# Kernel tuning notes

Hardware: AMD Instinct MI355X
Metric: run time of the kernel (lower is better)

The kernel has to match this reference:

```python
import jax, jax.numpy as jnp
import numpy as np

BN_EPS = 1e-5


def setup_inputs() -> dict:
    key = jax.random.key(0)
    ks = jax.random.split(key, 6)
    b, c_out, c_high = 8, 256, 512
    h1 = w1 = 64
    h2 = w2 = 32
    return {
        "fms_low": jax.random.normal(ks[0], (b, c_out, h1, w1), jnp.float32),
        "fms_high": jax.random.normal(ks[1], (b, c_high, h2, w2), jnp.float32),
        "w_conv": jax.random.normal(ks[2], (c_out, c_high), jnp.float32) * (1.0 / np.sqrt(c_high)),
        "bn_gamma": jnp.ones((c_out,), jnp.float32),
        "bn_beta": jnp.zeros((c_out,), jnp.float32),
        "bn_mean": jnp.zeros((c_out,), jnp.float32),
        "bn_var": jnp.ones((c_out,), jnp.float32),
        "fc1_w": jax.random.normal(ks[3], (c_out // 4, c_out), jnp.float32) * (1.0 / np.sqrt(c_out)),
        "fc1_b": jnp.zeros((c_out // 4,), jnp.float32),
        "fc2_w": jax.random.normal(ks[4], (c_out // 4, c_out), jnp.float32) * (1.0 / np.sqrt(c_out)),
        "fc2_b": jnp.zeros((c_out // 4,), jnp.float32),
        "scale": jax.random.normal(ks[5], (1,), jnp.float32),
    }


def reference(fms_low, fms_high, w_conv, bn_gamma, bn_beta, bn_mean, bn_var,
              fc1_w, fc1_b, fc2_w, fc2_b, scale):
    b, c, h1, w1 = fms_low.shape
    # conv_high: 1x1 conv (no bias) + BN (inference) + ReLU
    x = jnp.einsum('bchw,oc->bohw', fms_high, w_conv)  # [b, 256, h2, w2]
    inv = bn_gamma / jnp.sqrt(bn_var + BN_EPS)
    x = x * inv[None, :, None, None] + (bn_beta - bn_mean * inv)[None, :, None, None]
    x = jax.nn.relu(x)
    # raw row-major reshapes, matching torch .view(b, -1, C)
    feat_low = fms_low.reshape(b, -1, c)    # [b, N_low, 256]
    feat_high = x.reshape(b, -1, c)         # [b, N_high, 256]
    mid_low = feat_low @ fc1_w.T + fc1_b    # [b, N_low, 64]
    mid_high = feat_high @ fc2_w.T + fc2_b  # [b, N_high, 64]
    energy = jnp.einsum('bnd,bmd->bnm', mid_low, mid_high)  # [b, N_low, N_high]
    attn = jax.nn.softmax(energy, axis=-1)
    # bmm(feat_high^T, attn^T) -> [b, 256, N_low]
    mid = jnp.einsum('bmc,bnm->bcn', feat_high, attn).reshape(b, c, h1, w1)
    return scale[0] * mid
```

## Files before the change

kernel.cpp:

```cpp
#include <hip/hip_runtime.h>
#include <hip/hip_bf16.h>

typedef __bf16 v8bf __attribute__((ext_vector_type(8)));
typedef float  v4f  __attribute__((ext_vector_type(4)));

typedef __attribute__((address_space(3))) void       lds_vd;
typedef __attribute__((address_space(1))) const void gbl_vd;

#define MFMA16(a, b, c) __builtin_amdgcn_mfma_f32_16x16x32_bf16(a, b, c, 0, 0, 0)

__device__ __forceinline__ void split_hl(float v, __bf16* h, __bf16* l) {
    __bf16 hh = (__bf16)v;
    *h = hh;
    *l = (__bf16)(v - (float)hh);
}

__device__ __forceinline__ int swz_idx(int row, int col) {
    return row * 64 + ((((col >> 3) ^ (row & 7))) << 3) + (col & 7);
}
__device__ __forceinline__ const __bf16* frag_ptr(const __bf16* base, int row, int g) {
    return base + row * 64 + ((g ^ (row & 7)) << 3);
}


__global__ __launch_bounds__(256) void k_conv(
    const float* __restrict__ FH, const float* __restrict__ W,
    const float* __restrict__ gamma, const float* __restrict__ beta,
    const float* __restrict__ mean, const float* __restrict__ var,
    __bf16* __restrict__ Xhi, __bf16* __restrict__ Xlo, __bf16* __restrict__ VT)
{
    __shared__ __align__(16) __bf16 Ah[64 * 64];
    __shared__ __align__(16) __bf16 Al[64 * 64];
    __shared__ __align__(16) __bf16 Bh[64 * 64];
    __shared__ __align__(16) __bf16 Bl[64 * 64];
    __shared__ float invl[64], shl[64];

    const int tid = threadIdx.x, lane = tid & 63, w = tid >> 6;
    const int l15 = lane & 15, quad = lane >> 4;
    const int u0 = blockIdx.x * 16, o0 = blockIdx.y * 64, b = blockIdx.z;
    const float* FHb = FH + (size_t)b * 524288;

    if (tid < 64) {
        const int o = o0 + tid;
        const float iv = gamma[o] * rsqrtf(var[o] + 1e-5f);
        invl[tid] = iv;
        shl[tid] = beta[o] - mean[o] * iv;
    }

    const int ao = tid >> 2, aseg = tid & 3;
    float wreg[16], freg[16];
    {
        const float* wp = W + (size_t)(o0 + ao) * 512 + aseg * 16;
        #pragma unroll
        for (int q = 0; q < 4; ++q) {
            float4 f = ((const float4*)wp)[q];
            wreg[4*q] = f.x; wreg[4*q+1] = f.y; wreg[4*q+2] = f.z; wreg[4*q+3] = f.w;
        }
        const float* fp = FHb + (size_t)lane * 1024 + w * 256 + u0;
        #pragma unroll
        for (int q = 0; q < 4; ++q) {
            float4 f = ((const float4*)fp)[q];
            freg[4*q] = f.x; freg[4*q+1] = f.y; freg[4*q+2] = f.z; freg[4*q+3] = f.w;
        }
    }

    v4f acc[2][2];
    #pragma unroll
    for (int i = 0; i < 2; ++i)
        #pragma unroll
        for (int j = 0; j < 2; ++j) { v4f z = {0.f,0.f,0.f,0.f}; acc[i][j] = z; }
    const int oh = w >> 1, nh = w & 1;

    for (int ch = 0; ch < 8; ++ch) {
        if (ch) __syncthreads();
        #pragma unroll
        for (int z = 0; z < 2; ++z) {
            v8bf hv, lv;
            #pragma unroll
            for (int e = 0; e < 8; ++e) {
                __bf16 h, l; split_hl(wreg[8*z + e], &h, &l);
                hv[e] = h; lv[e] = l;
            }
            const int gi = (2*aseg + z) ^ (ao & 7);
            *(v8bf*)(Ah + ao*64 + (gi << 3)) = hv;
            *(v8bf*)(Al + ao*64 + (gi << 3)) = lv;
        }
        #pragma unroll
        for (int ul = 0; ul < 16; ++ul) {
            __bf16 h, l; split_hl(freg[ul], &h, &l);
            const int idx = (w*16 + ul)*64 + (((lane >> 3) ^ (ul & 7)) << 3) + (lane & 7);
            Bh[idx] = h; Bl[idx] = l;
        }
        __syncthreads();
        if (ch < 7) {
            const int c1 = (ch + 1) * 64;
            const float* wp = W + (size_t)(o0 + ao) * 512 + c1 + aseg * 16;
            #pragma unroll
            for (int q = 0; q < 4; ++q) {
                float4 f = ((const float4*)wp)[q];
                wreg[4*q] = f.x; wreg[4*q+1] = f.y; wreg[4*q+2] = f.z; wreg[4*q+3] = f.w;
            }
            const float* fp = FHb + (size_t)(c1 + lane) * 1024 + w * 256 + u0;
            #pragma unroll
            for (int q = 0; q < 4; ++q) {
                float4 f = ((const float4*)fp)[q];
                freg[4*q] = f.x; freg[4*q+1] = f.y; freg[4*q+2] = f.z; freg[4*q+3] = f.w;
            }
        }
        #pragma unroll
        for (int ks = 0; ks < 2; ++ks) {
            const int g = 4*ks + quad;
            v8bf a_h[2], a_l[2], b_h[2], b_l[2];
            #pragma unroll
            for (int i = 0; i < 2; ++i) {
                const int row = oh*32 + i*16 + l15;
                a_h[i] = *(const v8bf*)frag_ptr(Ah, row, g);
                a_l[i] = *(const v8bf*)frag_ptr(Al, row, g);
            }
            #pragma unroll
            for (int j = 0; j < 2; ++j) {
                const int row = nh*32 + j*16 + l15;
                b_h[j] = *(const v8bf*)frag_ptr(Bh, row, g);
                b_l[j] = *(const v8bf*)frag_ptr(Bl, row, g);
            }
            #pragma unroll
            for (int i = 0; i < 2; ++i)
                #pragma unroll
                for (int j = 0; j < 2; ++j) {
                    acc[i][j] = MFMA16(a_h[i], b_h[j], acc[i][j]);
                    acc[i][j] = MFMA16(a_h[i], b_l[j], acc[i][j]);
                    acc[i][j] = MFMA16(a_l[i], b_h[j], acc[i][j]);
                }
        }
    }
    __syncthreads();

    #pragma unroll
    for (int i = 0; i < 2; ++i)
        #pragma unroll
        for (int j = 0; j < 2; ++j)
            #pragma unroll
            for (int r = 0; r < 4; ++r) {
                const int row = oh*32 + i*16 + quad*4 + r;
                const int col = nh*32 + j*16 + l15;
                float v = acc[i][j][r] * invl[row] + shl[row];
                v = fmaxf(v, 0.f);
                __bf16 h, l; split_hl(v, &h, &l);
                const int idx = swz_idx(row, col);
                Ah[idx] = h; Al[idx] = l;
            }
    __syncthreads();
    {
        const int o = tid >> 2, pv = tid & 3;
        const size_t gbase = ((size_t)b*256 + o0 + o) * 1024 + pv*256 + u0;
        #pragma unroll
        for (int z = 0; z < 2; ++z) {
            const int gi = (2*pv + z) ^ (o & 7);
            v8bf h = *(v8bf*)(Ah + o*64 + (gi << 3));
            v8bf l = *(v8bf*)(Al + o*64 + (gi << 3));
            *(v8bf*)(Xhi + gbase + z*8) = h;
            *(v8bf*)(Xlo + gbase + z*8) = l;
        }
    }
    {
        const int ul = tid >> 4, s = tid & 15;
        __bf16 tmp[16];
        #pragma unroll
        for (int k = 0; k < 16; ++k) {
            const int m = s*16 + k;
            const int row = m >> 2;
            const int col = (m & 3)*16 + ul;
            tmp[k] = Ah[swz_idx(row, col)];
        }
        __bf16* vp = VT + ((size_t)b*256 + u0 + ul) * 1024 + 4*o0 + s*16;
        *(v8bf*)(vp)     = *(v8bf*)(tmp);
        *(v8bf*)(vp + 8) = *(v8bf*)(tmp + 8);
    }
}

__global__ __launch_bounds__(256) void k_proj32(
    const float* __restrict__ Feat, const float* __restrict__ Wfc,
    const float* __restrict__ bfc,
    __bf16* __restrict__ Ohi, __bf16* __restrict__ Olo)
{
    __shared__ __align__(16) __bf16 Ah[128 * 64], Al[128 * 64];
    __shared__ __align__(16) __bf16 Bh[64 * 64],  Bl[64 * 64];
    const int tid = threadIdx.x, lane = tid & 63, w = tid >> 6;
    const int l15 = lane & 15, quad = lane >> 4;
    const int r0 = blockIdx.x * 128;
    const int arow = tid >> 1, ahalf = tid & 1;
    const int brow = tid >> 2, bseg = tid & 3;

    float areg[32], breg[16];
    {
        const float* ap = Feat + (size_t)(r0 + arow) * 256 + ahalf * 32;
        #pragma unroll
        for (int q = 0; q < 8; ++q) {
            float4 f = ((const float4*)ap)[q];
            areg[4*q] = f.x; areg[4*q+1] = f.y; areg[4*q+2] = f.z; areg[4*q+3] = f.w;
        }
        const float* bp = Wfc + (size_t)brow * 256 + bseg * 16;
        #pragma unroll
        for (int q = 0; q < 4; ++q) {
            float4 f = ((const float4*)bp)[q];
            breg[4*q] = f.x; breg[4*q+1] = f.y; breg[4*q+2] = f.z; breg[4*q+3] = f.w;
        }
    }
    v4f acc[2][4];
    #pragma unroll
    for (int i = 0; i < 2; ++i)
        #pragma unroll
        for (int j = 0; j < 4; ++j) { v4f z = {0.f,0.f,0.f,0.f}; acc[i][j] = z; }

    for (int ch = 0; ch < 4; ++ch) {
        if (ch) __syncthreads();
        #pragma unroll
        for (int z = 0; z < 4; ++z) {
            v8bf hv, lv;
            #pragma unroll
            for (int e = 0; e < 8; ++e) {
                __bf16 h, l; split_hl(areg[8*z + e], &h, &l);
                hv[e] = h; lv[e] = l;
            }
            const int gi = (4*ahalf + z) ^ (arow & 7);
            *(v8bf*)(Ah + arow*64 + (gi << 3)) = hv;
            *(v8bf*)(Al + arow*64 + (gi << 3)) = lv;
        }
        #pragma unroll
        for (int z = 0; z < 2; ++z) {
            v8bf hv, lv;
            #pragma unroll
            for (int e = 0; e < 8; ++e) {
                __bf16 h, l; split_hl(breg[8*z + e], &h, &l);
                hv[e] = h; lv[e] = l;
            }
            const int gi = (2*bseg + z) ^ (brow & 7);
            *(v8bf*)(Bh + brow*64 + (gi << 3)) = hv;
            *(v8bf*)(Bl + brow*64 + (gi << 3)) = lv;
        }
        __syncthreads();
        if (ch < 3) {
            const int c1 = (ch + 1) * 64;
            const float* ap = Feat + (size_t)(r0 + arow) * 256 + c1 + ahalf * 32;
            #pragma unroll
            for (int q = 0; q < 8; ++q) {
                float4 f = ((const float4*)ap)[q];
                areg[4*q] = f.x; areg[4*q+1] = f.y; areg[4*q+2] = f.z; areg[4*q+3] = f.w;
            }
            const float* bp = Wfc + (size_t)brow * 256 + c1 + bseg * 16;
            #pragma unroll
            for (int q = 0; q < 4; ++q) {
                float4 f = ((const float4*)bp)[q];
                breg[4*q] = f.x; breg[4*q+1] = f.y; breg[4*q+2] = f.z; breg[4*q+3] = f.w;
            }
        }
        #pragma unroll
        for (int ks = 0; ks < 2; ++ks) {
            const int g = 4*ks + quad;
            v8bf a_h[2], a_l[2], b_h[4], b_l[4];
            #pragma unroll
            for (int i = 0; i < 2; ++i) {
                const int row = w*32 + i*16 + l15;
                a_h[i] = *(const v8bf*)frag_ptr(Ah, row, g);
                a_l[i] = *(const v8bf*)frag_ptr(Al, row, g);
            }
            #pragma unroll
            for (int j = 0; j < 4; ++j) {
                const int row = j*16 + l15;
                b_h[j] = *(const v8bf*)frag_ptr(Bh, row, g);
                b_l[j] = *(const v8bf*)frag_ptr(Bl, row, g);
            }
            #pragma unroll
            for (int i = 0; i < 2; ++i)
                #pragma unroll
                for (int j = 0; j < 4; ++j) {
                    acc[i][j] = MFMA16(a_h[i], b_h[j], acc[i][j]);
                    acc[i][j] = MFMA16(a_h[i], b_l[j], acc[i][j]);
                    acc[i][j] = MFMA16(a_l[i], b_h[j], acc[i][j]);
                }
        }
    }
    __syncthreads();
    #pragma unroll
    for (int j = 0; j < 4; ++j) {
        const float bias = bfc[j*16 + l15];
        #pragma unroll
        for (int i = 0; i < 2; ++i)
            #pragma unroll
            for (int r = 0; r < 4; ++r) {
                const int row = w*32 + i*16 + quad*4 + r;
                const int col = j*16 + l15;
                __bf16 h, l; split_hl(acc[i][j][r] + bias, &h, &l);
                const int idx = swz_idx(row, col);
                Ah[idx] = h; Al[idx] = l;
            }
    }
    __syncthreads();
    {
        const int row = tid >> 1, half = tid & 1;
        __bf16* oh_ = Ohi + (size_t)(r0 + row) * 64 + half * 32;
        __bf16* ol_ = Olo + (size_t)(r0 + row) * 64 + half * 32;
        #pragma unroll
        for (int z = 0; z < 4; ++z) {
            const int gi = (4*half + z) ^ (row & 7);
            *(v8bf*)(oh_ + z*8) = *(v8bf*)(Ah + row*64 + (gi << 3));
            *(v8bf*)(ol_ + z*8) = *(v8bf*)(Al + row*64 + (gi << 3));
        }
    }
}

__global__ __launch_bounds__(256) void k_projbf(
    const __bf16* __restrict__ Fhi, const __bf16* __restrict__ Flo,
    const float* __restrict__ Wfc, const float* __restrict__ bfc,
    __bf16* __restrict__ Ohi, __bf16* __restrict__ Olo)
{
    __shared__ __align__(16) __bf16 Ah[32 * 64], Al[32 * 64];
    __shared__ __align__(16) __bf16 Bh[64 * 64], Bl[64 * 64];
    const int tid = threadIdx.x, lane = tid & 63, w = tid >> 6;
    const int l15 = lane & 15, quad = lane >> 4;
    const int r0 = blockIdx.x * 32;
    const int srow = tid >> 3, sg = tid & 7;
    const int brow = tid >> 2, bseg = tid & 3;

    float breg[16];
    v8bf ha, la;
    {
        ha = *(const v8bf*)(Fhi + (size_t)(r0 + srow) * 256 + sg * 8);
        la = *(const v8bf*)(Flo + (size_t)(r0 + srow) * 256 + sg * 8);
        const float* bp = Wfc + (size_t)brow * 256 + bseg * 16;
        #pragma unroll
        for (int q = 0; q < 4; ++q) {
            float4 f = ((const float4*)bp)[q];
            breg[4*q] = f.x; breg[4*q+1] = f.y; breg[4*q+2] = f.z; breg[4*q+3] = f.w;
        }
    }
    v4f acc[2];
    { v4f z = {0.f,0.f,0.f,0.f}; acc[0] = z; acc[1] = z; }
    const int mt = w >> 1, nh = w & 1;

    for (int ch = 0; ch < 4; ++ch) {
        if (ch) __syncthreads();
        {
            const int gi = sg ^ (srow & 7);
            *(v8bf*)(Ah + srow*64 + (gi << 3)) = ha;
            *(v8bf*)(Al + srow*64 + (gi << 3)) = la;
        }
        #pragma unroll
        for (int z = 0; z < 2; ++z) {
            v8bf hv, lv;
            #pragma unroll
            for (int e = 0; e < 8; ++e) {
                __bf16 h, l; split_hl(breg[8*z + e], &h, &l);
                hv[e] = h; lv[e] = l;
            }
            const int gi = (2*bseg + z) ^ (brow & 7);
            *(v8bf*)(Bh + brow*64 + (gi << 3)) = hv;
            *(v8bf*)(Bl + brow*64 + (gi << 3)) = lv;
        }
        __syncthreads();
        if (ch < 3) {
            const int c1 = (ch + 1) * 64;
            ha = *(const v8bf*)(Fhi + (size_t)(r0 + srow) * 256 + c1 + sg * 8);
            la = *(const v8bf*)(Flo + (size_t)(r0 + srow) * 256 + c1 + sg * 8);
            const float* bp = Wfc + (size_t)brow * 256 + c1 + bseg * 16;
            #pragma unroll
            for (int q = 0; q < 4; ++q) {
                float4 f = ((const float4*)bp)[q];
                breg[4*q] = f.x; breg[4*q+1] = f.y; breg[4*q+2] = f.z; breg[4*q+3] = f.w;
            }
        }
        #pragma unroll
        for (int ks = 0; ks < 2; ++ks) {
            const int g = 4*ks + quad;
            const int arow = mt*16 + l15;
            v8bf a_h = *(const v8bf*)frag_ptr(Ah, arow, g);
            v8bf a_l = *(const v8bf*)frag_ptr(Al, arow, g);
            #pragma unroll
            for (int j = 0; j < 2; ++j) {
                const int row = (nh*2 + j)*16 + l15;
                v8bf b_h = *(const v8bf*)frag_ptr(Bh, row, g);
                v8bf b_l = *(const v8bf*)frag_ptr(Bl, row, g);
                acc[j] = MFMA16(a_h, b_h, acc[j]);
                acc[j] = MFMA16(a_h, b_l, acc[j]);
                acc[j] = MFMA16(a_l, b_h, acc[j]);
            }
        }
    }
    __syncthreads();
    #pragma unroll
    for (int j = 0; j < 2; ++j) {
        const float bias = bfc[(nh*2 + j)*16 + l15];
        #pragma unroll
        for (int r = 0; r < 4; ++r) {
            const int row = mt*16 + quad*4 + r;
            const int col = (nh*2 + j)*16 + l15;
            __bf16 h, l; split_hl(acc[j][r] + bias, &h, &l);
            const int idx = swz_idx(row, col);
            Ah[idx] = h; Al[idx] = l;
        }
    }
    __syncthreads();
    {
        const int row = tid >> 3, g = tid & 7;
        const int gi = g ^ (row & 7);
        *(v8bf*)(Ohi + (size_t)(r0 + row) * 64 + g*8) = *(v8bf*)(Ah + row*64 + (gi << 3));
        *(v8bf*)(Olo + (size_t)(r0 + row) * 64 + g*8) = *(v8bf*)(Al + row*64 + (gi << 3));
    }
}

__global__ __launch_bounds__(256, 2) void k_attn(
    const __bf16* __restrict__ MLhi, const __bf16* __restrict__ MLlo,
    const __bf16* __restrict__ MHhi, const __bf16* __restrict__ MHlo,
    const __bf16* __restrict__ VT,
    const float* __restrict__ scale_p,
    float* __restrict__ out)
{
    __shared__ __align__(16) __bf16 Khi[2][32 * 64];
    __shared__ __align__(16) __bf16 Klo[2][32 * 64];
    __shared__ __align__(16) __bf16 Vs [2][256 * 32];
    __shared__ __align__(16) __bf16 Ps [4][16 * 32];
    __shared__ float lsh[4][16];

    const int tid = threadIdx.x, lane = tid & 63, w = tid >> 6;
    const int l15 = lane & 15, quad = lane >> 4;
    const int b = blockIdx.x & 7, qtb = blockIdx.x >> 3;
    const int q0 = qtb * 64;

    v8bf qhi[2], qlo[2];
    {
        const __bf16* qp  = MLhi + ((size_t)(b*4096 + q0 + w*16 + l15)) * 64;
        const __bf16* qlp = MLlo + ((size_t)(b*4096 + q0 + w*16 + l15)) * 64;
        #pragma unroll
        for (int h = 0; h < 2; ++h) {
            qhi[h] = *(const v8bf*)(qp + h*32 + quad*8);
            qlo[h] = *(const v8bf*)(qlp + h*32 + quad*8);
        }
    }

    const char* Khg = (const char*)(MHhi + (size_t)b * 65536);
    const char* Klg = (const char*)(MHlo + (size_t)b * 65536);
    const char* Vg  = (const char*)(VT + (size_t)b * 262144);
    const int offK = (lane >> 3) * 128 + (((lane & 7) ^ ((lane >> 3) & 7)) << 4);
    const int offV = (lane >> 2) * 2048 + ((((lane & 3) ^ ((lane >> 3) & 3))) << 4);

    v4f oacc[4][4];
    #pragma unroll
    for (int qt = 0; qt < 4; ++qt)
        #pragma unroll
        for (int cb = 0; cb < 4; ++cb) { v4f z = {0.f,0.f,0.f,0.f}; oacc[qt][cb] = z; }
    float lrow[4] = {0.f, 0.f, 0.f, 0.f};

    {
        __builtin_amdgcn_global_load_lds((gbl_vd*)(Khg + w*1024 + offK),
                                         (lds_vd*)((char*)&Khi[0][0] + w*1024), 16, 0, 0);
        __builtin_amdgcn_global_load_lds((gbl_vd*)(Klg + w*1024 + offK),
                                         (lds_vd*)((char*)&Klo[0][0] + w*1024), 16, 0, 0);
        #pragma unroll
        for (int i = w; i < 16; i += 4)
            __builtin_amdgcn_global_load_lds((gbl_vd*)(Vg + i*32768 + offV),
                                             (lds_vd*)((char*)&Vs[0][0] + i*1024), 16, 0, 0);
    }

    for (int ch = 0; ch < 32; ++ch) {
        const int cur = ch & 1;
        const __bf16* Kh = &Khi[cur][0];
        const __bf16* Kl = &Klo[cur][0];
        const __bf16* Vc = &Vs[cur][0];

        __syncthreads();

        if (ch < 31) {
            const int m0n = (ch + 1) * 32;
            const int nb = cur ^ 1;
            __builtin_amdgcn_global_load_lds((gbl_vd*)(Khg + m0n*128 + w*1024 + offK),
                                             (lds_vd*)((char*)&Khi[nb][0] + w*1024), 16, 0, 0);
            __builtin_amdgcn_global_load_lds((gbl_vd*)(Klg + m0n*128 + w*1024 + offK),
                                             (lds_vd*)((char*)&Klo[nb][0] + w*1024), 16, 0, 0);
            #pragma unroll
            for (int i = w; i < 16; i += 4)
                __builtin_amdgcn_global_load_lds((gbl_vd*)(Vg + m0n*2 + i*32768 + offV),
                                                 (lds_vd*)((char*)&Vs[nb][0] + i*1024), 16, 0, 0);
        }

        float S[2][4];
        __builtin_amdgcn_s_setprio(1);
        #pragma unroll
        for (int mb = 0; mb < 2; ++mb) {
            v4f sacc = {0.f, 0.f, 0.f, 0.f};
            #pragma unroll
            for (int h = 0; h < 2; ++h) {
                const int row = mb*16 + l15, g = 4*h + quad;
                v8bf kh = *(const v8bf*)frag_ptr(Kh, row, g);
                v8bf kl = *(const v8bf*)frag_ptr(Kl, row, g);
                sacc = MFMA16(qhi[h], kh, sacc);
                sacc = MFMA16(qhi[h], kl, sacc);
                sacc = MFMA16(qlo[h], kh, sacc);
            }
            #pragma unroll
            for (int r = 0; r < 4; ++r) S[mb][r] = sacc[r];
        }
        __builtin_amdgcn_s_setprio(0);

        #pragma unroll
        for (int mb = 0; mb < 2; ++mb)
            #pragma unroll
            for (int r = 0; r < 4; ++r) {
                const float p = __expf(S[mb][r]);
                S[mb][r] = p;
                lrow[r] += p;
            }
        #pragma unroll
        for (int mb = 0; mb < 2; ++mb)
            #pragma unroll
            for (int r = 0; r < 4; ++r) {
                const int row = quad*4 + r;
                const int slot = (mb*2 + (l15 >> 3)) ^ ((row >> 1) & 3);
                Ps[w][row*32 + (slot << 3) + (l15 & 7)] = (__bf16)S[mb][r];
            }
        asm volatile("s_waitcnt lgkmcnt(0)\n\ts_barrier" ::: "memory");

        v8bf pa[4];
        #pragma unroll
        for (int qt = 0; qt < 4; ++qt)
            pa[qt] = *(const v8bf*)(Ps[qt] + l15*32 + ((quad ^ ((l15 >> 1) & 3)) << 3));
        __builtin_amdgcn_s_setprio(1);
        #pragma unroll
        for (int cb = 0; cb < 4; ++cb) {
            const int vrow = w*64 + cb*16 + l15;
            v8bf vv = *(const v8bf*)(Vc + vrow*32 + ((quad ^ ((vrow >> 1) & 3)) << 3));
            #pragma unroll
            for (int qt = 0; qt < 4; ++qt)
                oacc[qt][cb] = MFMA16(pa[qt], vv, oacc[qt][cb]);
        }
        __builtin_amdgcn_s_setprio(0);
    }

    #pragma unroll
    for (int r = 0; r < 4; ++r) {
        float s = lrow[r];
        #pragma unroll
        for (int d = 1; d < 16; d <<= 1) s += __shfl_xor(s, d, 64);
        lrow[r] = s;
    }
    if (l15 == 0) {
        #pragma unroll
        for (int r = 0; r < 4; ++r) lsh[w][quad*4 + r] = lrow[r];
    }
    __syncthreads();

    const float scl = scale_p[0];
    float inv[4][4];
    #pragma unroll
    for (int qt = 0; qt < 4; ++qt)
        #pragma unroll
        for (int r = 0; r < 4; ++r) inv[qt][r] = scl / lsh[qt][quad*4 + r];
    float* outb = out + (size_t)b * 256 * 4096;
    #pragma unroll
    for (int cb = 0; cb < 4; ++cb) {
        const int c = w*64 + cb*16 + l15;
        #pragma unroll
        for (int qt = 0; qt < 4; ++qt) {
            float4 v;
            v.x = oacc[qt][cb][0] * inv[qt][0];
            v.y = oacc[qt][cb][1] * inv[qt][1];
            v.z = oacc[qt][cb][2] * inv[qt][2];
            v.w = oacc[qt][cb][3] * inv[qt][3];
            *(float4*)(outb + (size_t)c * 4096 + q0 + qt*16 + quad*4) = v;
        }
    }
}

extern "C" void kernel_launch(void* const* d_in, const int* in_sizes, int n_in,
                              void* d_out, int out_size, void* d_ws, size_t ws_size,
                              hipStream_t stream)
{
    const float* fms_low  = (const float*)d_in[0];
    const float* fms_high = (const float*)d_in[1];
    const float* w_conv   = (const float*)d_in[2];
    const float* gamma    = (const float*)d_in[3];
    const float* beta     = (const float*)d_in[4];
    const float* mean     = (const float*)d_in[5];
    const float* var      = (const float*)d_in[6];
    const float* fc1_w    = (const float*)d_in[7];
    const float* fc1_b    = (const float*)d_in[8];
    const float* fc2_w    = (const float*)d_in[9];
    const float* fc2_b    = (const float*)d_in[10];
    const float* scale    = (const float*)d_in[11];
    float* out = (float*)d_out;

    __bf16* Xhi  = (__bf16*)d_ws;
    __bf16* Xlo  = Xhi  + (size_t)8*256*1024;
    __bf16* VT   = Xlo  + (size_t)8*256*1024;
    __bf16* MLhi = VT   + (size_t)8*256*1024;
    __bf16* MLlo = MLhi + (size_t)8*4096*64;
    __bf16* MHhi = MLlo + (size_t)8*4096*64;
    __bf16* MHlo = MHhi + (size_t)8*1024*64;

    k_conv<<<dim3(16, 4, 8), 256, 0, stream>>>(fms_high, w_conv, gamma, beta,
                                               mean, var, Xhi, Xlo, VT);
    k_projbf<<<dim3(256), 256, 0, stream>>>(Xhi, Xlo, fc2_w, fc2_b, MHhi, MHlo);
    k_proj32<<<dim3(256), 256, 0, stream>>>(fms_low, fc1_w, fc1_b, MLhi, MLlo);
    k_attn<<<dim3(512), 256, 0, stream>>>(MLhi, MLlo, MHhi, MHlo, VT, scale, out);
}
```

Measured before the change: 186.4 us.

## Split attention block across eight waves and software-pipeline QK with PV

The attention kernel now runs 512 threads per block: each wave computes one 16x16 score tile (query tile by key half) instead of two, and the PV stage splits the 256 channels across eight waves. The P buffer is double-buffered so the PV product for the previous chunk overlaps with the QK scores and exp of the current chunk, which removes one barrier per iteration. Row sums are combined from two halves at the end. This raises waves per block and per-wave parallelism, at the cost of more LDS for P, an extra pipeline stage and one redundant final prefetch.

```diff
diff --git a/kernel.cpp b/kernel.cpp
--- a/kernel.cpp
+++ b/kernel.cpp
@@ -408,7 +408,7 @@
     }
 }
 
-__global__ __launch_bounds__(256, 2) void k_attn(
+__global__ __launch_bounds__(512, 4) void k_attn(
     const __bf16* __restrict__ MLhi, const __bf16* __restrict__ MLlo,
     const __bf16* __restrict__ MHhi, const __bf16* __restrict__ MHlo,
     const __bf16* __restrict__ VT,
@@ -418,23 +418,29 @@
     __shared__ __align__(16) __bf16 Khi[2][32 * 64];
     __shared__ __align__(16) __bf16 Klo[2][32 * 64];
     __shared__ __align__(16) __bf16 Vs [2][256 * 32];
-    __shared__ __align__(16) __bf16 Ps [4][16 * 32];
-    __shared__ float lsh[4][16];
+    __shared__ __align__(16) __bf16 Ps [2][4][16 * 32];
+    __shared__ float lsh[2][4][16];
 
     const int tid = threadIdx.x, lane = tid & 63, w = tid >> 6;
     const int l15 = lane & 15, quad = lane >> 4;
     const int b = blockIdx.x & 7, qtb = blockIdx.x >> 3;
     const int q0 = qtb * 64;
+    const int qt = w & 3, mb = w >> 2;
 
     v8bf qhi[2], qlo[2];
     {
-        const __bf16* qp  = MLhi + ((size_t)(b*4096 + q0 + w*16 + l15)) * 64;
-        const __bf16* qlp = MLlo + ((size_t)(b*4096 + q0 + w*16 + l15)) * 64;
+        const __bf16* qp  = MLhi + ((size_t)(b*4096 + q0 + qt*16 + l15)) * 64;
+        const __bf16* qlp = MLlo + ((size_t)(b*4096 + q0 + qt*16 + l15)) * 64;
         #pragma unroll
         for (int h = 0; h < 2; ++h) {
             qhi[h] = *(const v8bf*)(qp + h*32 + quad*8);
             qlo[h] = *(const v8bf*)(qlp + h*32 + quad*8);
         }
+    }
+    #pragma unroll
+    for (int h = 0; h < 2; ++h) {
+        asm volatile("" : "+v"(qhi[h]));
+        asm volatile("" : "+v"(qlo[h]));
     }
 
     const char* Khg = (const char*)(MHhi + (size_t)b * 65536);
@@ -443,96 +449,103 @@
     const int offK = (lane >> 3) * 128 + (((lane & 7) ^ ((lane >> 3) & 7)) << 4);
     const int offV = (lane >> 2) * 2048 + ((((lane & 3) ^ ((lane >> 3) & 3))) << 4);
 
-    v4f oacc[4][4];
-    #pragma unroll
-    for (int qt = 0; qt < 4; ++qt)
-        #pragma unroll
-        for (int cb = 0; cb < 4; ++cb) { v4f z = {0.f,0.f,0.f,0.f}; oacc[qt][cb] = z; }
+    const char* kgsrc = (w < 4) ? Khg : Klg;
+    const int ksub = (w & 3) * 1024;
+
+    v4f oacc[4][2];
+    #pragma unroll
+    for (int t = 0; t < 4; ++t)
+        #pragma unroll
+        for (int cb = 0; cb < 2; ++cb) { v4f z = {0.f,0.f,0.f,0.f}; oacc[t][cb] = z; }
     float lrow[4] = {0.f, 0.f, 0.f, 0.f};
 
     {
-        __builtin_amdgcn_global_load_lds((gbl_vd*)(Khg + w*1024 + offK),
-                                         (lds_vd*)((char*)&Khi[0][0] + w*1024), 16, 0, 0);
-        __builtin_amdgcn_global_load_lds((gbl_vd*)(Klg + w*1024 + offK),
-                                         (lds_vd*)((char*)&Klo[0][0] + w*1024), 16, 0, 0);
-        #pragma unroll
-        for (int i = w; i < 16; i += 4)
+        char* kdst = (char*)((w < 4) ? &Khi[0][0] : &Klo[0][0]);
+        __builtin_amdgcn_global_load_lds((gbl_vd*)(kgsrc + ksub + offK),
+                                         (lds_vd*)(kdst + ksub), 16, 0, 0);
+        #pragma unroll
+        for (int j = 0; j < 2; ++j) {
+            const int i = w*2 + j;
             __builtin_amdgcn_global_load_lds((gbl_vd*)(Vg + i*32768 + offV),
                                              (lds_vd*)((char*)&Vs[0][0] + i*1024), 16, 0, 0);
-    }
+        }
+    }
+    asm volatile("s_waitcnt vmcnt(2)\n\ts_barrier" ::: "memory");
 
     for (int ch = 0; ch < 32; ++ch) {
-        const int cur = ch & 1;
-        const __bf16* Kh = &Khi[cur][0];
-        const __bf16* Kl = &Klo[cur][0];
-        const __bf16* Vc = &Vs[cur][0];
-
-        __syncthreads();
-
-        if (ch < 31) {
-            const int m0n = (ch + 1) * 32;
-            const int nb = cur ^ 1;
-            __builtin_amdgcn_global_load_lds((gbl_vd*)(Khg + m0n*128 + w*1024 + offK),
-                                             (lds_vd*)((char*)&Khi[nb][0] + w*1024), 16, 0, 0);
-            __builtin_amdgcn_global_load_lds((gbl_vd*)(Klg + m0n*128 + w*1024 + offK),
-                                             (lds_vd*)((char*)&Klo[nb][0] + w*1024), 16, 0, 0);
-            #pragma unroll
-            for (int i = w; i < 16; i += 4)
-                __builtin_amdgcn_global_load_lds((gbl_vd*)(Vg + m0n*2 + i*32768 + offV),
-                                                 (lds_vd*)((char*)&Vs[nb][0] + i*1024), 16, 0, 0);
-        }
-
-        float S[2][4];
+        const int cur = ch & 1, nxt = cur ^ 1;
+        const int mn = ((ch < 31) ? (ch + 1) : 31) * 32;
+
+        {
+            char* kdst = (char*)((w < 4) ? &Khi[nxt][0] : &Klo[nxt][0]);
+            __builtin_amdgcn_global_load_lds((gbl_vd*)(kgsrc + mn*128 + ksub + offK),
+                                             (lds_vd*)(kdst + ksub), 16, 0, 0);
+        }
+
+        v4f sacc = {0.f, 0.f, 0.f, 0.f};
         __builtin_amdgcn_s_setprio(1);
         #pragma unroll
-        for (int mb = 0; mb < 2; ++mb) {
-            v4f sacc = {0.f, 0.f, 0.f, 0.f};
-            #pragma unroll
-            for (int h = 0; h < 2; ++h) {
-                const int row = mb*16 + l15, g = 4*h + quad;
-                v8bf kh = *(const v8bf*)frag_ptr(Kh, row, g);
-                v8bf kl = *(const v8bf*)frag_ptr(Kl, row, g);
-                sacc = MFMA16(qhi[h], kh, sacc);
-                sacc = MFMA16(qhi[h], kl, sacc);
-                sacc = MFMA16(qlo[h], kh, sacc);
-            }
-            #pragma unroll
-            for (int r = 0; r < 4; ++r) S[mb][r] = sacc[r];
+        for (int h = 0; h < 2; ++h) {
+            const int row = mb*16 + l15, g = 4*h + quad;
+            v8bf kh = *(const v8bf*)frag_ptr(&Khi[cur][0], row, g);
+            v8bf kl = *(const v8bf*)frag_ptr(&Klo[cur][0], row, g);
+            sacc = MFMA16(qhi[h], kh, sacc);
+            sacc = MFMA16(qhi[h], kl, sacc);
+            sacc = MFMA16(qlo[h], kh, sacc);
         }
         __builtin_amdgcn_s_setprio(0);
 
         #pragma unroll
-        for (int mb = 0; mb < 2; ++mb)
-            #pragma unroll
-            for (int r = 0; r < 4; ++r) {
-                const float p = __expf(S[mb][r]);
-                S[mb][r] = p;
-                lrow[r] += p;
-            }
-        #pragma unroll
-        for (int mb = 0; mb < 2; ++mb)
-            #pragma unroll
-            for (int r = 0; r < 4; ++r) {
-                const int row = quad*4 + r;
-                const int slot = (mb*2 + (l15 >> 3)) ^ ((row >> 1) & 3);
-                Ps[w][row*32 + (slot << 3) + (l15 & 7)] = (__bf16)S[mb][r];
-            }
-        asm volatile("s_waitcnt lgkmcnt(0)\n\ts_barrier" ::: "memory");
-
+        for (int r = 0; r < 4; ++r) {
+            const float p = __expf(sacc[r]);
+            lrow[r] += p;
+            const int row = quad*4 + r;
+            const int slot = (mb*2 + (l15 >> 3)) ^ ((row >> 1) & 3);
+            Ps[cur][qt][row*32 + (slot << 3) + (l15 & 7)] = (__bf16)p;
+        }
+
+        if (ch) {
+            const int pb = nxt;
+            v8bf pa[4];
+            #pragma unroll
+            for (int t = 0; t < 4; ++t)
+                pa[t] = *(const v8bf*)(&Ps[pb][t][0] + l15*32 + ((quad ^ ((l15 >> 1) & 3)) << 3));
+            __builtin_amdgcn_s_setprio(1);
+            #pragma unroll
+            for (int cb = 0; cb < 2; ++cb) {
+                const int vrow = w*32 + cb*16 + l15;
+                v8bf vv = *(const v8bf*)(&Vs[pb][0] + vrow*32 + ((quad ^ ((vrow >> 1) & 3)) << 3));
+                #pragma unroll
+                for (int t = 0; t < 4; ++t)
+                    oacc[t][cb] = MFMA16(pa[t], vv, oacc[t][cb]);
+            }
+            __builtin_amdgcn_s_setprio(0);
+        }
+
+        asm volatile("s_waitcnt lgkmcnt(0)" ::: "memory");
+        #pragma unroll
+        for (int j = 0; j < 2; ++j) {
+            const int i = w*2 + j;
+            __builtin_amdgcn_global_load_lds((gbl_vd*)(Vg + mn*2 + i*32768 + offV),
+                                             (lds_vd*)((char*)&Vs[nxt][0] + i*1024), 16, 0, 0);
+        }
+
+        asm volatile("s_waitcnt vmcnt(2) lgkmcnt(0)\n\ts_barrier" ::: "memory");
+    }
+
+    {
         v8bf pa[4];
         #pragma unroll
-        for (int qt = 0; qt < 4; ++qt)
-            pa[qt] = *(const v8bf*)(Ps[qt] + l15*32 + ((quad ^ ((l15 >> 1) & 3)) << 3));
-        __builtin_amdgcn_s_setprio(1);
-        #pragma unroll
-        for (int cb = 0; cb < 4; ++cb) {
-            const int vrow = w*64 + cb*16 + l15;
-            v8bf vv = *(const v8bf*)(Vc + vrow*32 + ((quad ^ ((vrow >> 1) & 3)) << 3));
-            #pragma unroll
-            for (int qt = 0; qt < 4; ++qt)
-                oacc[qt][cb] = MFMA16(pa[qt], vv, oacc[qt][cb]);
-        }
-        __builtin_amdgcn_s_setprio(0);
+        for (int t = 0; t < 4; ++t)
+            pa[t] = *(const v8bf*)(&Ps[1][t][0] + l15*32 + ((quad ^ ((l15 >> 1) & 3)) << 3));
+        #pragma unroll
+        for (int cb = 0; cb < 2; ++cb) {
+            const int vrow = w*32 + cb*16 + l15;
+            v8bf vv = *(const v8bf*)(&Vs[1][0] + vrow*32 + ((quad ^ ((vrow >> 1) & 3)) << 3));
+            #pragma unroll
+            for (int t = 0; t < 4; ++t)
+                oacc[t][cb] = MFMA16(pa[t], vv, oacc[t][cb]);
+        }
     }
 
     #pragma unroll
@@ -544,28 +557,29 @@
     }
     if (l15 == 0) {
         #pragma unroll
-        for (int r = 0; r < 4; ++r) lsh[w][quad*4 + r] = lrow[r];
+        for (int r = 0; r < 4; ++r) lsh[mb][qt][quad*4 + r] = lrow[r];
     }
     __syncthreads();
 
     const float scl = scale_p[0];
     float inv[4][4];
     #pragma unroll
-    for (int qt = 0; qt < 4; ++qt)
-        #pragma unroll
-        for (int r = 0; r < 4; ++r) inv[qt][r] = scl / lsh[qt][quad*4 + r];
+    for (int t = 0; t < 4; ++t)
+        #pragma unroll
+        for (int r = 0; r < 4; ++r)
+            inv[t][r] = scl / (lsh[0][t][quad*4 + r] + lsh[1][t][quad*4 + r]);
     float* outb = out + (size_t)b * 256 * 4096;
     #pragma unroll
-    for (int cb = 0; cb < 4; ++cb) {
-        const int c = w*64 + cb*16 + l15;
-        #pragma unroll
-        for (int qt = 0; qt < 4; ++qt) {
+    for (int cb = 0; cb < 2; ++cb) {
+        const int c = w*32 + cb*16 + l15;
+        #pragma unroll
+        for (int t = 0; t < 4; ++t) {
             float4 v;
-            v.x = oacc[qt][cb][0] * inv[qt][0];
-            v.y = oacc[qt][cb][1] * inv[qt][1];
-            v.z = oacc[qt][cb][2] * inv[qt][2];
-            v.w = oacc[qt][cb][3] * inv[qt][3];
-            *(float4*)(outb + (size_t)c * 4096 + q0 + qt*16 + quad*4) = v;
+            v.x = oacc[t][cb][0] * inv[t][0];
+            v.y = oacc[t][cb][1] * inv[t][1];
+            v.z = oacc[t][cb][2] * inv[t][2];
+            v.w = oacc[t][cb][3] * inv[t][3];
+            *(float4*)(outb + (size_t)c * 4096 + q0 + t*16 + quad*4) = v;
         }
     }
 }
@@ -600,5 +614,5 @@
                                                mean, var, Xhi, Xlo, VT);
     k_projbf<<<dim3(256), 256, 0, stream>>>(Xhi, Xlo, fc2_w, fc2_b, MHhi, MHlo);
     k_proj32<<<dim3(256), 256, 0, stream>>>(fms_low, fc1_w, fc1_b, MLhi, MLlo);
-    k_attn<<<dim3(512), 256, 0, stream>>>(MLhi, MLlo, MHhi, MHlo, VT, scale, out);
-}
+    k_attn<<<dim3(512), 512, 0, stream>>>(MLhi, MLlo, MHhi, MHlo, VT, scale, out);
+}
```

After: 184.0 us. Within noise of the previous version (-1.3%).
